# Kernel tuning notes

Hardware: AMD Instinct MI355X
Metric: run time of the kernel (lower is better)

Reference implementation:

```python
import jax, jax.numpy as jnp
import numpy as np


def _ssm_layer(x, A, B, C, bias):
    # x: [Bt, T, D]; diagonal linear recurrence s_t = sigmoid(A)*s_{t-1} + B*x_t; y_t = C*s_t + bias
    a = jax.nn.sigmoid(A)

    def step(s, xt):
        s = a * s + B * xt
        return s, C * s + bias

    xT = jnp.swapaxes(x, 0, 1)  # [T, Bt, D]
    s0 = jnp.zeros(x.shape[::2], dtype=x.dtype)  # [Bt, D]
    _, yT = jax.lax.scan(step, s0, xT)
    return jnp.swapaxes(yT, 0, 1)  # [Bt, T, D]


def setup_inputs() -> dict:
    key = jax.random.key(0)
    ks = jax.random.split(key, 6)
    Bt, T, F, H, L = 8, 4096, 512, 1024, 4
    x = jax.random.normal(ks[0], (Bt, T, F), dtype=jnp.float32)
    W_in = jax.random.normal(ks[1], (F, H), dtype=jnp.float32) * (1.0 / np.sqrt(F))
    b_in = jnp.zeros((H,), dtype=jnp.float32)
    A = jax.random.uniform(ks[2], (L, H), dtype=jnp.float32)  # torch.rand init
    B = jax.random.normal(ks[3], (L, H), dtype=jnp.float32)
    C = jax.random.normal(ks[4], (L, H), dtype=jnp.float32)
    bias = jnp.zeros((L, H), dtype=jnp.float32)
    return {"x": x, "W_in": W_in, "b_in": b_in, "A": A, "B": B, "C": C, "bias": bias}


def reference(x, W_in, b_in, A, B, C, bias):
    # in_proj (dropout is identity at p=0)
    y = jnp.einsum('btf,fh->bth', x, W_in) + b_in
    n_layers = A.shape[0]
    for l in range(n_layers):  # small fixed layer count
        y = _ssm_layer(y, A[l], B[l], C[l], bias[l])
    # return_sequence=True, unidirectional -> y: [B, T, H]
    return y
```

## Files before the change

kernel.cpp:

```cpp
#include <hip/hip_runtime.h>
#include <hip/hip_bf16.h>
#include <stdint.h>

#define BT     8
#define T_SEQ  4096
#define K_F    512
#define N_H    1024
#define M_TOT  (BT * T_SEQ)
#define NLAYER 4
#define LC     32
#define NC     (T_SEQ / LC)

typedef short  bf16x8 __attribute__((ext_vector_type(8)));
typedef float  f32x4  __attribute__((ext_vector_type(4)));
typedef ushort u16x8  __attribute__((ext_vector_type(8)));
typedef ushort u16x4  __attribute__((ext_vector_type(4)));

__device__ __forceinline__ ushort f2bf(float f) {
  uint32_t u = __builtin_bit_cast(uint32_t, f);
  u += 0x7fffu + ((u >> 16) & 1u);
  return (ushort)(u >> 16);
}
__device__ __forceinline__ float bf2f(ushort u) {
  uint32_t x = (uint32_t)u << 16;
  return __builtin_bit_cast(float, x);
}

__device__ __forceinline__ void gload16(const void* g, void* l) {
  __builtin_amdgcn_global_load_lds(
      (const __attribute__((address_space(1))) uint32_t*)g,
      (__attribute__((address_space(3))) uint32_t*)l, 16, 0, 0);
}

#define CVT_BLOCKS ((M_TOT * K_F) / (256 * 8))

__global__ __launch_bounds__(256) void prep_kernel(const float* __restrict__ x,
                                                   ushort* __restrict__ xb,
                                                   const float* __restrict__ W,
                                                   ushort* __restrict__ Wt) {
  __shared__ float tile[32][33];
  const int bid = blockIdx.x;
  if (bid < CVT_BLOCKS) {
    const int i = bid * 256 + threadIdx.x;
    const float4* xv = (const float4*)x;
    float4 v0 = xv[2 * i + 0];
    float4 v1 = xv[2 * i + 1];
    u16x8 o;
    o[0] = f2bf(v0.x); o[1] = f2bf(v0.y); o[2] = f2bf(v0.z); o[3] = f2bf(v0.w);
    o[4] = f2bf(v1.x); o[5] = f2bf(v1.y); o[6] = f2bf(v1.z); o[7] = f2bf(v1.w);
    *((u16x8*)xb + i) = o;
  } else {
    const int idx = bid - CVT_BLOCKS;
    const int k0 = (idx & 15) * 32;
    const int n0 = (idx >> 4) * 32;
    const int lx = threadIdx.x & 31;
    const int ly = threadIdx.x >> 5;
#pragma unroll
    for (int j = 0; j < 32; j += 8)
      tile[ly + j][lx] = W[(size_t)(k0 + ly + j) * N_H + n0 + lx];
    __syncthreads();
#pragma unroll
    for (int j = 0; j < 32; j += 8)
      Wt[(size_t)(n0 + ly + j) * K_F + k0 + lx] = f2bf(tile[lx][ly + j]);
  }
}

#define BM 128
#define BN 128
#define BKK 64

__global__ __launch_bounds__(256) void gemm_kernel(
    const ushort* __restrict__ Xb, const ushort* __restrict__ Wt,
    const float* __restrict__ bias, ushort* __restrict__ Yb,
    const float* __restrict__ As, const float* __restrict__ Bs,
    const float* __restrict__ Cs, const float* __restrict__ Ds,
    float* __restrict__ E) {
  __shared__ ushort lds[BM * BKK * 2];
  ushort* lsA = lds;
  ushort* lsB = lds + BM * BKK;
  const int tid  = threadIdx.x;
  const int lane = tid & 63;
  const int wv   = tid >> 6;
  const int wr   = wv >> 1;
  const int wc   = wv & 1;
  const int m0   = blockIdx.x * BM;
  const int n0   = blockIdx.y * BN;

  const int srow = (lane >> 3);
  const int scol = (lane & 7) * 8;
  const ushort* gA = Xb + (size_t)m0 * K_F + scol;
  const ushort* gB = Wt + (size_t)n0 * K_F + scol;

  f32x4 acc[4][4];
#pragma unroll
  for (int i = 0; i < 4; i++)
#pragma unroll
    for (int j = 0; j < 4; j++) acc[i][j] = (f32x4)0.0f;

  const int lr = lane & 15;
  const int kg = (lane >> 4) * 8;

  for (int kt = 0; kt < K_F; kt += BKK) {
#pragma unroll
    for (int i = 0; i < 4; i++) {
      const int reg = wv * 4 + i;
      const int r   = reg * 8 + srow;
      gload16(gA + (size_t)r * K_F + kt, &lsA[reg * 512]);
      gload16(gB + (size_t)r * K_F + kt, &lsB[reg * 512]);
    }
    __syncthreads();

    bf16x8 af[4][2], bfr[4][2];
#pragma unroll
    for (int fm = 0; fm < 4; fm++)
#pragma unroll
      for (int kk = 0; kk < 2; kk++)
        af[fm][kk] = *(const bf16x8*)&lsA[(wr * 64 + fm * 16 + lr) * BKK + kk * 32 + kg];
#pragma unroll
    for (int fn = 0; fn < 4; fn++)
#pragma unroll
      for (int kk = 0; kk < 2; kk++)
        bfr[fn][kk] = *(const bf16x8*)&lsB[(wc * 64 + fn * 16 + lr) * BKK + kk * 32 + kg];

#pragma unroll
    for (int kk = 0; kk < 2; kk++)
#pragma unroll
      for (int fm = 0; fm < 4; fm++)
#pragma unroll
        for (int fn = 0; fn < 4; fn++)
          acc[fm][fn] = __builtin_amdgcn_mfma_f32_16x16x32_bf16(af[fm][kk], bfr[fn][kk],
                                                                acc[fm][fn], 0, 0, 0);
    __syncthreads();
  }

#pragma unroll
  for (int fn = 0; fn < 4; fn++) {
    const int col = wc * 64 + fn * 16 + lr;
    const float bv = bias[n0 + col];
#pragma unroll
    for (int fm = 0; fm < 4; fm++) {
      const int row0 = wr * 64 + fm * 16 + (lane >> 4) * 4;
#pragma unroll
      for (int i = 0; i < 4; i++)
        lds[(row0 + i) * BN + col] = f2bf(acc[fm][fn][i] + bv);
    }
  }
  __syncthreads();

  const int erow = tid >> 4;
  const int ecol = (tid & 15) * 8;
#pragma unroll
  for (int p = 0; p < 8; p++) {
    const int row = p * 16 + erow;
    u16x8 v = *(const u16x8*)&lds[row * BN + ecol];
    *(u16x8*)&Yb[(size_t)(m0 + row) * N_H + n0 + ecol] = v;
  }

  {
    const int bidx = m0 >> 12;
    const int c0   = (m0 & (T_SEQ - 1)) >> 5;
    const int hl   = tid & 127;
    const int ck0  = tid >> 7;
    const int h    = n0 + hl;

    float a[4], bb[4], cc[4], dd[4];
#pragma unroll
    for (int l = 0; l < 4; l++) {
      a[l]  = 1.f / (1.f + __expf(-As[l * N_H + h]));
      bb[l] = Bs[l * N_H + h];
      cc[l] = Cs[l * N_H + h];
      dd[l] = Ds[l * N_H + h];
    }

#pragma unroll
    for (int p = 0; p < 2; p++) {
      const int ck = ck0 + p * 2;
      float s[4] = {0.f, 0.f, 0.f, 0.f};
#pragma unroll 4
      for (int t = 0; t < LC; t++) {
        float xv = bf2f(lds[(ck * LC + t) * BN + hl]);
#pragma unroll
        for (int l = 0; l < 4; l++) {
          s[l] = fmaf(a[l], s[l], bb[l] * xv);
          xv = fmaf(cc[l], s[l], dd[l]);
        }
      }
      f32x4 e;
      e[0] = s[0]; e[1] = s[1]; e[2] = s[2]; e[3] = s[3];
      ((f32x4*)E)[(size_t)(bidx * NC + c0 + ck) * N_H + h] = e;
    }
  }
}

__global__ __launch_bounds__(256) void chunk_scan_kernel(
    const float* __restrict__ A, const float* __restrict__ B,
    const float* __restrict__ C, const float* __restrict__ E,
    float* __restrict__ S) {
  const int idx = blockIdx.x * 256 + threadIdx.x;
  const int b = idx >> 10;
  const int h = idx & (N_H - 1);

  float a[4], bcoef[4], ccoef[4];
#pragma unroll
  for (int l = 0; l < 4; l++) {
    a[l] = 1.f / (1.f + __expf(-A[l * N_H + h]));
    bcoef[l] = B[l * N_H + h];
    ccoef[l] = C[l * N_H + h];
  }

  float m[4][4] = {};
  m[0][0] = a[0];
  m[1][0] = bcoef[1] * ccoef[0] * a[0];
  m[1][1] = a[1];
  m[2][0] = bcoef[2] * ccoef[1] * m[1][0];
  m[2][1] = bcoef[2] * ccoef[1] * a[1];
  m[2][2] = a[2];
  m[3][0] = bcoef[3] * ccoef[2] * m[2][0];
  m[3][1] = bcoef[3] * ccoef[2] * m[2][1];
  m[3][2] = bcoef[3] * ccoef[2] * a[2];
  m[3][3] = a[3];

#pragma unroll
  for (int it = 0; it < 5; it++) {
    float t[4][4];
#pragma unroll
    for (int i = 0; i < 4; i++)
#pragma unroll
      for (int j = 0; j < 4; j++) {
        float acc = 0.f;
#pragma unroll
        for (int k = 0; k < 4; k++) acc = fmaf(m[i][k], m[k][j], acc);
        t[i][j] = acc;
      }
#pragma unroll
    for (int i = 0; i < 4; i++)
#pragma unroll
      for (int j = 0; j < 4; j++) m[i][j] = t[i][j];
  }

  float s[4] = {0.f, 0.f, 0.f, 0.f};
  const f32x4* Ep = (const f32x4*)E + (size_t)b * NC * N_H + h;
  f32x4* Sp = (f32x4*)S + (size_t)b * NC * N_H + h;
#pragma unroll 4
  for (int c = 0; c < NC; c++) {
    f32x4 sv;
    sv[0] = s[0]; sv[1] = s[1]; sv[2] = s[2]; sv[3] = s[3];
    Sp[(size_t)c * N_H] = sv;
    f32x4 e = Ep[(size_t)c * N_H];
    float ns[4];
#pragma unroll
    for (int i = 0; i < 4; i++) {
      float acc = e[i];
#pragma unroll
      for (int k = 0; k < 4; k++) acc = fmaf(m[i][k], s[k], acc);
      ns[i] = acc;
    }
#pragma unroll
    for (int i = 0; i < 4; i++) s[i] = ns[i];
  }
}

__global__ __launch_bounds__(256) void chunk_apply_kernel(
    const ushort* __restrict__ Yb, float* __restrict__ out,
    const float* __restrict__ A, const float* __restrict__ B,
    const float* __restrict__ C, const float* __restrict__ D,
    const float* __restrict__ S) {
  const int b  = blockIdx.x / NC;
  const int c  = blockIdx.x % NC;
  const int h4 = threadIdx.x << 2;

  float a[4][4], bb[4][4], cc[4][4], dd[4][4];
#pragma unroll
  for (int l = 0; l < 4; l++) {
    f32x4 av = *(const f32x4*)(A + l * N_H + h4);
    f32x4 bv = *(const f32x4*)(B + l * N_H + h4);
    f32x4 cv = *(const f32x4*)(C + l * N_H + h4);
    f32x4 dv = *(const f32x4*)(D + l * N_H + h4);
#pragma unroll
    for (int ch = 0; ch < 4; ch++) {
      a[l][ch]  = 1.f / (1.f + __expf(-av[ch]));
      bb[l][ch] = bv[ch]; cc[l][ch] = cv[ch]; dd[l][ch] = dv[ch];
    }
  }

  float s[4][4];
  const f32x4* sp = (const f32x4*)S + (size_t)(b * NC + c) * N_H + h4;
#pragma unroll
  for (int ch = 0; ch < 4; ch++) {
    f32x4 sv = sp[ch];
    s[0][ch] = sv[0]; s[1][ch] = sv[1]; s[2][ch] = sv[2]; s[3][ch] = sv[3];
  }

  const ushort* ybase = Yb + ((size_t)b * T_SEQ + (size_t)c * LC) * N_H + h4;
  f32x4* op = (f32x4*)(out + ((size_t)b * T_SEQ + (size_t)c * LC) * N_H) + (h4 >> 2);
#pragma unroll 4
  for (int t = 0; t < LC; t++) {
    u16x4 xv = *(const u16x4*)(ybase + (size_t)t * N_H);
    f32x4 ov;
#pragma unroll
    for (int ch = 0; ch < 4; ch++) {
      float x = bf2f(xv[ch]);
#pragma unroll
      for (int l = 0; l < 4; l++) {
        s[l][ch] = fmaf(a[l][ch], s[l][ch], bb[l][ch] * x);
        x = fmaf(cc[l][ch], s[l][ch], dd[l][ch]);
      }
      ov[ch] = x;
    }
    __builtin_nontemporal_store(ov, op + (size_t)t * (N_H / 4));
  }
}

extern "C" void kernel_launch(void* const* d_in, const int* in_sizes, int n_in,
                              void* d_out, int out_size, void* d_ws, size_t ws_size,
                              hipStream_t stream) {
  const float* x    = (const float*)d_in[0];
  const float* W    = (const float*)d_in[1];
  const float* b_in = (const float*)d_in[2];
  const float* A    = (const float*)d_in[3];
  const float* B    = (const float*)d_in[4];
  const float* C    = (const float*)d_in[5];
  const float* bias = (const float*)d_in[6];
  float* out = (float*)d_out;

  char* wsb = (char*)d_ws;
  ushort* xb = (ushort*)wsb;
  ushort* Wt = (ushort*)(wsb + (size_t)33 * 1024 * 1024 - (size_t)N_H * K_F * 2);
  ushort* Yb = (ushort*)(wsb + (size_t)40 * 1024 * 1024);
  float*  E  = (float*)(wsb + (size_t)112 * 1024 * 1024);
  float*  S  = E + (size_t)BT * NC * N_H * 4;

  prep_kernel<<<CVT_BLOCKS + 512, 256, 0, stream>>>(x, xb, W, Wt);
  gemm_kernel<<<dim3(M_TOT / BM, N_H / BN), 256, 0, stream>>>(xb, Wt, b_in, Yb,
                                                              A, B, C, bias, E);
  chunk_scan_kernel<<<(BT * N_H) / 256, 256, 0, stream>>>(A, B, C, E, S);
  chunk_apply_kernel<<<BT * NC, 256, 0, stream>>>(Yb, out, A, B, C, bias, S);
}
```

Baseline: 145.9 us.

## Double-buffer GEMM LDS tiles with K-step 32 and prefetch next stage

Splits the LDS into two buffers and issues the global-to-LDS loads for the next K tile before computing on the current one, so the load latency overlaps the MFMA work. The K tile shrinks from 64 to 32 to keep the LDS footprint at 32KB. This leaves one barrier per iteration instead of two, but doubles the iteration count and halves the MFMA work between barriers. Correctness depends on gload16 being an async direct-to-LDS load that completes before the following barrier.

Result: faster. 136.0 us (-6.8%).

```diff
diff --git a/kernel.cpp b/kernel.cpp
--- a/kernel.cpp
+++ b/kernel.cpp
@@ -67,7 +67,8 @@
 
 #define BM 128
 #define BN 128
-#define BKK 64
+#define BKK 32
+#define NKT (K_F / BKK)
 
 __global__ __launch_bounds__(256) void gemm_kernel(
     const ushort* __restrict__ Xb, const ushort* __restrict__ Wt,
@@ -75,9 +76,7 @@
     const float* __restrict__ As, const float* __restrict__ Bs,
     const float* __restrict__ Cs, const float* __restrict__ Ds,
     float* __restrict__ E) {
-  __shared__ ushort lds[BM * BKK * 2];
-  ushort* lsA = lds;
-  ushort* lsB = lds + BM * BKK;
+  __shared__ ushort lds[16384];
   const int tid  = threadIdx.x;
   const int lane = tid & 63;
   const int wv   = tid >> 6;
@@ -86,10 +85,10 @@
   const int m0   = blockIdx.x * BM;
   const int n0   = blockIdx.y * BN;
 
-  const int srow = (lane >> 3);
-  const int scol = (lane & 7) * 8;
-  const ushort* gA = Xb + (size_t)m0 * K_F + scol;
-  const ushort* gB = Wt + (size_t)n0 * K_F + scol;
+  const int arow = lane >> 2;
+  const int acol = (lane & 3) * 8;
+  const ushort* gA = Xb + (size_t)m0 * K_F + acol;
+  const ushort* gB = Wt + (size_t)n0 * K_F + acol;
 
   f32x4 acc[4][4];
 #pragma unroll
@@ -100,38 +99,44 @@
   const int lr = lane & 15;
   const int kg = (lane >> 4) * 8;
 
-  for (int kt = 0; kt < K_F; kt += BKK) {
-#pragma unroll
-    for (int i = 0; i < 4; i++) {
-      const int reg = wv * 4 + i;
-      const int r   = reg * 8 + srow;
-      gload16(gA + (size_t)r * K_F + kt, &lsA[reg * 512]);
-      gload16(gB + (size_t)r * K_F + kt, &lsB[reg * 512]);
-    }
+#define STAGE(kt, buf)                                                        \
+  do {                                                                        \
+    ushort* _a = &lds[(buf) * 8192];                                          \
+    ushort* _b = &lds[(buf) * 8192 + 4096];                                   \
+    _Pragma("unroll")                                                         \
+    for (int _i = 0; _i < 2; _i++) {                                          \
+      const int _r = wv * 2 + _i;                            \
+      gload16(gA + (size_t)(_r * 16 + arow) * K_F + (kt) * BKK, &_a[_r * 512]); \
+      gload16(gB + (size_t)(_r * 16 + arow) * K_F + (kt) * BKK, &_b[_r * 512]); \
+    }                                                                         \
+  } while (0)
+
+  STAGE(0, 0);
+  __syncthreads();
+
+  for (int kt = 0; kt < NKT; kt++) {
+    const int buf = kt & 1;
+    if (kt + 1 < NKT) STAGE(kt + 1, buf ^ 1);
+
+    const ushort* la = &lds[buf * 8192];
+    const ushort* lb = &lds[buf * 8192 + 4096];
+    bf16x8 af[4], bfr[4];
+#pragma unroll
+    for (int fm = 0; fm < 4; fm++)
+      af[fm] = *(const bf16x8*)&la[(wr * 64 + fm * 16 + lr) * BKK + kg];
+#pragma unroll
+    for (int fn = 0; fn < 4; fn++)
+      bfr[fn] = *(const bf16x8*)&lb[(wc * 64 + fn * 16 + lr) * BKK + kg];
+
+#pragma unroll
+    for (int fm = 0; fm < 4; fm++)
+#pragma unroll
+      for (int fn = 0; fn < 4; fn++)
+        acc[fm][fn] = __builtin_amdgcn_mfma_f32_16x16x32_bf16(af[fm], bfr[fn],
+                                                              acc[fm][fn], 0, 0, 0);
     __syncthreads();
-
-    bf16x8 af[4][2], bfr[4][2];
-#pragma unroll
-    for (int fm = 0; fm < 4; fm++)
-#pragma unroll
-      for (int kk = 0; kk < 2; kk++)
-        af[fm][kk] = *(const bf16x8*)&lsA[(wr * 64 + fm * 16 + lr) * BKK + kk * 32 + kg];
-#pragma unroll
-    for (int fn = 0; fn < 4; fn++)
-#pragma unroll
-      for (int kk = 0; kk < 2; kk++)
-        bfr[fn][kk] = *(const bf16x8*)&lsB[(wc * 64 + fn * 16 + lr) * BKK + kk * 32 + kg];
-
-#pragma unroll
-    for (int kk = 0; kk < 2; kk++)
-#pragma unroll
-      for (int fm = 0; fm < 4; fm++)
-#pragma unroll
-        for (int fn = 0; fn < 4; fn++)
-          acc[fm][fn] = __builtin_amdgcn_mfma_f32_16x16x32_bf16(af[fm][kk], bfr[fn][kk],
-                                                                acc[fm][fn], 0, 0, 0);
-    __syncthreads();
-  }
+  }
+#undef STAGE
 
 #pragma unroll
   for (int fn = 0; fn < 4; fn++) {
```
